# Performance work log

Measured on AMD Instinct MI355X. Metric: run time of the kernel, lower is better.

## Reference

```python
import jax, jax.numpy as jnp
import numpy as np

NEG_SLOPE = 0.2

def _leaky_relu(x):
    return jnp.where(x >= 0, x, NEG_SLOPE * x)

def setup_inputs() -> dict:
    key = jax.random.key(0)
    ks = jax.random.split(key, 12)
    B, N, M = 64, 4096, 128
    d_ope, d_ma, d_out = 6, 3, 8
    return {
        "ope_ma_adj": jax.random.randint(ks[0], (B, N, M), 0, 2, dtype=jnp.int32),
        "batch_idxes": jnp.arange(B, dtype=jnp.int32),
        "ope_feat": jax.random.normal(ks[1], (B, N, d_ope), dtype=jnp.float32),
        "ma_feat": jax.random.normal(ks[2], (B, M, d_ma), dtype=jnp.float32),
        "proc_time": jax.random.uniform(ks[3], (B, N, M), dtype=jnp.float32),
        "W_src": jax.random.normal(ks[4], (d_ope, d_out), dtype=jnp.float32),
        "W_dst": jax.random.normal(ks[5], (d_ma, d_out), dtype=jnp.float32),
        "w_edge": jax.random.normal(ks[6], (d_out,), dtype=jnp.float32),
        "attn_l": jax.random.normal(ks[7], (d_out,), dtype=jnp.float32),
        "attn_r": jax.random.normal(ks[8], (d_out,), dtype=jnp.float32),
        "attn_e": jax.random.normal(ks[9], (d_out,), dtype=jnp.float32),
    }

def reference(ope_ma_adj, batch_idxes, ope_feat, ma_feat, proc_time,
              W_src, W_dst, w_edge, attn_l, attn_r, attn_e):
    # GATedge.forward with num_head=1 (head dim folded away).
    adj_i = ope_ma_adj[batch_idxes]            # [B,N,M] int (0/1)
    adj = adj_i.astype(jnp.float32)
    feat_src = ope_feat @ W_src                # [B,N,d]
    feat_dst = ma_feat @ W_dst                 # [B,M,d]
    el = feat_src @ attn_l                     # [B,N]
    er = feat_dst @ attn_r                     # [B,M]
    # fc_edge is Linear(1,d): feat_edge = proc[...,None]*w_edge, so
    # ee = (feat_edge*attn_e).sum(-1) = proc * dot(w_edge, attn_e)
    ee = proc_time * jnp.dot(w_edge, attn_e)   # [B,N,M]
    a = adj * el[:, :, None] + ee + adj * er[:, None, :]
    eijk = _leaky_relu(a)                      # [B,N,M]
    ekk = _leaky_relu(2.0 * er)                # [B,M]
    neg_inf = jnp.asarray(-jnp.inf, dtype=eijk.dtype)
    eijk_m = jnp.where(adj_i == 1, eijk, neg_inf)
    e = jnp.concatenate([eijk_m, ekk[:, None, :]], axis=1)   # [B,N+1,M]
    alpha = jax.nn.softmax(e, axis=1)          # softmax over ops (+self)
    alpha_ijk = alpha[:, :-1, :]               # [B,N,M]
    alpha_kk = alpha[:, -1, :]                 # [B,M]
    # b = sum_j alpha_ijk * (feat_edge + feat_src), split to avoid [B,N,M,d]
    b_edge = jnp.einsum('bnm,bnm->bm', alpha_ijk, proc_time)[..., None] * w_edge  # [B,M,d]
    b_src = jnp.einsum('bnm,bnd->bmd', alpha_ijk, feat_src)                       # [B,M,d]
    c = feat_dst * alpha_kk[..., None]         # [B,M,d]
    return jax.nn.sigmoid(b_edge + b_src + c)  # nu_k_prime [B,M,d]
```

## Files before the change

### kernel.cpp

```cpp
#include <hip/hip_runtime.h>
#include <hip/hip_bf16.h>

constexpr int B  = 64;
constexpr int N  = 4096;
constexpr int M  = 128;
constexpr int DO = 8;
constexpr int NC = 32;
constexpr int CH = N / NC;
constexpr int RW = CH / 4;
constexpr int NS = RW / 2;
constexpr float CEXP = 20.0f;

constexpr int waitimm(int n) { return (n & 15) | ((n >> 4) << 14) | (7 << 4) | (15 << 8); }

typedef __attribute__((address_space(3))) void       lds_void;
typedef const __attribute__((address_space(1))) void gbl_void;

__global__ __launch_bounds__(256) void hgnn_k1(
    const int*   __restrict__ adj,
    const int*   __restrict__ bidx,
    const float* __restrict__ ope_feat,
    const float* __restrict__ ma_feat,
    const float* __restrict__ proc,
    const float* __restrict__ W_src,
    const float* __restrict__ W_dst,
    const float* __restrict__ w_edge,
    const float* __restrict__ attn_l,
    const float* __restrict__ attn_r,
    const float* __restrict__ attn_e,
    float*       __restrict__ acc)
{
    const int chunk = blockIdx.x;
    const int b     = blockIdx.y;
    const int t     = threadIdx.x;
    const int w     = t >> 6;
    const int lane  = t & 63;
    const int n0    = chunk * CH;

    __shared__ __align__(16) int   bufA[4][4][256];
    __shared__ __align__(16) float bufP[4][4][256];
    __shared__ __align__(16) float fs[CH][DO];
    __shared__ float el_s[CH];

    const int c0 = lane;
    const int c1 = lane + 64;

    float er0 = 0.f, er1 = 0.f, cee = 0.f;
    {
        const float* mf0 = ma_feat + ((size_t)b * M + c0) * 3;
        const float* mf1 = ma_feat + ((size_t)b * M + c1) * 3;
        const float a0 = mf0[0], a1 = mf0[1], a2 = mf0[2];
        const float b0 = mf1[0], b1 = mf1[1], b2 = mf1[2];
#pragma unroll
        for (int d = 0; d < DO; ++d) {
            er0 += (a0 * W_dst[d] + a1 * W_dst[DO + d] + a2 * W_dst[2 * DO + d]) * attn_r[d];
            er1 += (b0 * W_dst[d] + b1 * W_dst[DO + d] + b2 * W_dst[2 * DO + d]) * attn_r[d];
            cee += w_edge[d] * attn_e[d];
        }
    }

    if (t < CH) {
        const float* of = ope_feat + ((size_t)b * N + (n0 + t)) * 6;
        const float o0 = of[0], o1 = of[1], o2 = of[2], o3 = of[3], o4 = of[4], o5 = of[5];
        float el = 0.f;
#pragma unroll
        for (int d = 0; d < DO; ++d) {
            const float f = o0 * W_src[d] + o1 * W_src[DO + d] + o2 * W_src[2 * DO + d] +
                            o3 * W_src[3 * DO + d] + o4 * W_src[4 * DO + d] + o5 * W_src[5 * DO + d];
            fs[t][d] = f;
            el += f * attn_l[d];
        }
        el_s[t] = el;
    }
    __syncthreads();

    const int ab = bidx[b];
    const int*   adjw  = adj  + ((size_t)ab * N + n0 + w * RW) * M;
    const float* procw = proc + ((size_t)b  * N + n0 + w * RW) * M;
    const int l4 = lane * 4;

    auto issue = [&](int S) {
        __builtin_amdgcn_global_load_lds((gbl_void*)(adjw + (size_t)S * 256 + l4),
                                         (lds_void*)&bufA[w][S & 3][0], 16, 0, 0);
        __builtin_amdgcn_global_load_lds((gbl_void*)(procw + (size_t)S * 256 + l4),
                                         (lds_void*)&bufP[w][S & 3][0], 16, 0, 0);
    };

    float l0 = 0.f, sp0 = 0.f, l1 = 0.f, sp1 = 0.f;
    float sf0[DO], sf1[DO];
#pragma unroll
    for (int d = 0; d < DO; ++d) { sf0[d] = 0.f; sf1[d] = 0.f; }

    auto consume = [&](int S) {
        const int sb = (S & 3) * 256;
        const int* bA = &bufA[w][0][0];
        const float* bP = &bufP[w][0][0];
#pragma unroll
        for (int rr = 0; rr < 2; ++rr) {
            const int r = w * RW + S * 2 + rr;
            const float  el = el_s[r];
            const float4 f0 = *reinterpret_cast<const float4*>(&fs[r][0]);
            const float4 f1 = *reinterpret_cast<const float4*>(&fs[r][4]);
            const int   a0 = bA[sb + rr * 128 + c0];
            const int   a1 = bA[sb + rr * 128 + c1];
            const float p0 = bP[sb + rr * 128 + c0];
            const float p1 = bP[sb + rr * 128 + c1];
            {
                float v = el + er0 + cee * p0;
                v = (v >= 0.f) ? v : 0.2f * v;
                const float wt = __expf(((a0 != 0) ? v : -1e30f) - CEXP);
                l0 += wt; sp0 = fmaf(wt, p0, sp0);
                sf0[0] = fmaf(wt, f0.x, sf0[0]); sf0[1] = fmaf(wt, f0.y, sf0[1]);
                sf0[2] = fmaf(wt, f0.z, sf0[2]); sf0[3] = fmaf(wt, f0.w, sf0[3]);
                sf0[4] = fmaf(wt, f1.x, sf0[4]); sf0[5] = fmaf(wt, f1.y, sf0[5]);
                sf0[6] = fmaf(wt, f1.z, sf0[6]); sf0[7] = fmaf(wt, f1.w, sf0[7]);
            }
            {
                float v = el + er1 + cee * p1;
                v = (v >= 0.f) ? v : 0.2f * v;
                const float wt = __expf(((a1 != 0) ? v : -1e30f) - CEXP);
                l1 += wt; sp1 = fmaf(wt, p1, sp1);
                sf1[0] = fmaf(wt, f0.x, sf1[0]); sf1[1] = fmaf(wt, f0.y, sf1[1]);
                sf1[2] = fmaf(wt, f0.z, sf1[2]); sf1[3] = fmaf(wt, f0.w, sf1[3]);
                sf1[4] = fmaf(wt, f1.x, sf1[4]); sf1[5] = fmaf(wt, f1.y, sf1[5]);
                sf1[6] = fmaf(wt, f1.z, sf1[6]); sf1[7] = fmaf(wt, f1.w, sf1[7]);
            }
        }
    };

    issue(0); issue(1); issue(2); issue(3);

#define STEP_MI(S) { __builtin_amdgcn_s_waitcnt(waitimm(6)); consume(S); issue((S) + 4); }
#define STEP_NI(S, WN) { __builtin_amdgcn_s_waitcnt(waitimm(WN)); consume(S); }
    STEP_MI(0)  STEP_MI(1)  STEP_MI(2)  STEP_MI(3)
    STEP_MI(4)  STEP_MI(5)  STEP_MI(6)  STEP_MI(7)
    STEP_MI(8)  STEP_MI(9)  STEP_MI(10) STEP_MI(11)
    STEP_NI(12, 6) STEP_NI(13, 4) STEP_NI(14, 2) STEP_NI(15, 0)
#undef STEP_MI
#undef STEP_NI

    float* R = reinterpret_cast<float*>(&bufA[0][0][0]);
    const size_t colbase = (size_t)b * M;

    __syncthreads();
    {
        float v0[5] = {l0, sp0, sf0[0], sf0[1], sf0[2]};
        float v1[5] = {l1, sp1, sf1[0], sf1[1], sf1[2]};
#pragma unroll
        for (int k = 0; k < 5; ++k) {
            R[(w * 5 + k) * 128 + c0] = v0[k];
            R[(w * 5 + k) * 128 + c1] = v1[k];
        }
    }
    __syncthreads();
    if (t < M) {
#pragma unroll
        for (int k = 0; k < 5; ++k) {
            const float s = R[(0 * 5 + k) * 128 + t] + R[(1 * 5 + k) * 128 + t] +
                            R[(2 * 5 + k) * 128 + t] + R[(3 * 5 + k) * 128 + t];
            atomicAdd(&acc[(size_t)k * (B * M) + colbase + t], s);
        }
    }
    __syncthreads();
    {
        float v0[5] = {sf0[3], sf0[4], sf0[5], sf0[6], sf0[7]};
        float v1[5] = {sf1[3], sf1[4], sf1[5], sf1[6], sf1[7]};
#pragma unroll
        for (int k = 0; k < 5; ++k) {
            R[(w * 5 + k) * 128 + c0] = v0[k];
            R[(w * 5 + k) * 128 + c1] = v1[k];
        }
    }
    __syncthreads();
    if (t < M) {
#pragma unroll
        for (int k = 0; k < 5; ++k) {
            const float s = R[(0 * 5 + k) * 128 + t] + R[(1 * 5 + k) * 128 + t] +
                            R[(2 * 5 + k) * 128 + t] + R[(3 * 5 + k) * 128 + t];
            atomicAdd(&acc[(size_t)(5 + k) * (B * M) + colbase + t], s);
        }
    }
}

__global__ __launch_bounds__(256) void hgnn_k2(
    const float* __restrict__ ma_feat,
    const float* __restrict__ W_dst,
    const float* __restrict__ w_edge,
    const float* __restrict__ attn_r,
    const float* __restrict__ acc,
    float*       __restrict__ out)
{
    const int t = blockIdx.x * 256 + threadIdx.x;
    if (t >= B * M) return;
    const int m = t & (M - 1);
    const int b = t >> 7;

    float a[10];
#pragma unroll
    for (int f = 0; f < 10; ++f) a[f] = acc[(size_t)f * (B * M) + t];

    const float* mf = ma_feat + ((size_t)b * M + m) * 3;
    const float f0 = mf[0], f1 = mf[1], f2 = mf[2];
    float fd[DO];
    float er = 0.f;
#pragma unroll
    for (int d = 0; d < DO; ++d) {
        fd[d] = f0 * W_dst[d] + f1 * W_dst[DO + d] + f2 * W_dst[2 * DO + d];
        er += fd[d] * attn_r[d];
    }
    float ekk = 2.f * er;
    ekk = (ekk >= 0.f) ? ekk : 0.2f * ekk;
    const float wkk = __expf(ekk - CEXP);

    const float L    = a[0] + wkk;
    const float invL = 1.f / L;
    const float akk  = wkk * invL;
    const float spf  = a[1] * invL;

#pragma unroll
    for (int d = 0; d < DO; ++d) {
        const float x = spf * w_edge[d] + a[2 + d] * invL + fd[d] * akk;
        out[(size_t)t * DO + d] = 1.f / (1.f + __expf(-x));
    }
}

extern "C" void kernel_launch(void* const* d_in, const int* in_sizes, int n_in,
                              void* d_out, int out_size, void* d_ws, size_t ws_size,
                              hipStream_t stream) {
    const int*   adj      = (const int*)  d_in[0];
    const int*   bidx     = (const int*)  d_in[1];
    const float* ope_feat = (const float*)d_in[2];
    const float* ma_feat  = (const float*)d_in[3];
    const float* proc     = (const float*)d_in[4];
    const float* W_src    = (const float*)d_in[5];
    const float* W_dst    = (const float*)d_in[6];
    const float* w_edge   = (const float*)d_in[7];
    const float* attn_l   = (const float*)d_in[8];
    const float* attn_r   = (const float*)d_in[9];
    const float* attn_e   = (const float*)d_in[10];
    float* out = (float*)d_out;
    float* acc = (float*)d_ws;

    hipMemsetAsync(acc, 0, (size_t)10 * B * M * sizeof(float), stream);
    hgnn_k1<<<dim3(NC, B), 256, 0, stream>>>(adj, bidx, ope_feat, ma_feat, proc,
                                             W_src, W_dst, w_edge, attn_l, attn_r,
                                             attn_e, acc);
    hgnn_k2<<<dim3((B * M + 255) / 256), 256, 0, stream>>>(ma_feat, W_dst, w_edge,
                                                           attn_r, acc, out);
}
```

Before: 302.3 us.

## Replace LDS async staging with register-prefetched int2/float2 direct loads

Drops the global_load_lds ring buffer in LDS for adjacency and proc_time. Each lane now owns two adjacent columns and loads them as int2/float2 straight into registers, with a 4-deep software prefetch. This frees LDS and requests up to 8 blocks per CU via launch bounds, aiming for higher occupancy to hide memory latency. The masking is also simplified to select 0 after the exp, and leaky ReLU becomes fmaxf. The trade-off is narrower 8-byte loads per lane and more register pressure, where the old path used explicit 16-byte async copies.

```diff
diff --git a/kernel.cpp b/kernel.cpp
--- a/kernel.cpp
+++ b/kernel.cpp
@@ -1,5 +1,4 @@
 #include <hip/hip_runtime.h>
-#include <hip/hip_bf16.h>
 
 constexpr int B  = 64;
 constexpr int N  = 4096;
@@ -8,15 +7,10 @@
 constexpr int NC = 32;
 constexpr int CH = N / NC;
 constexpr int RW = CH / 4;
-constexpr int NS = RW / 2;
+constexpr int DP = 4;
 constexpr float CEXP = 20.0f;
 
-constexpr int waitimm(int n) { return (n & 15) | ((n >> 4) << 14) | (7 << 4) | (15 << 8); }
-
-typedef __attribute__((address_space(3))) void       lds_void;
-typedef const __attribute__((address_space(1))) void gbl_void;
-
-__global__ __launch_bounds__(256) void hgnn_k1(
+__global__ __launch_bounds__(256, 8) void hgnn_k1(
     const int*   __restrict__ adj,
     const int*   __restrict__ bidx,
     const float* __restrict__ ope_feat,
@@ -37,20 +31,17 @@
     const int lane  = t & 63;
     const int n0    = chunk * CH;
 
-    __shared__ __align__(16) int   bufA[4][4][256];
-    __shared__ __align__(16) float bufP[4][4][256];
     __shared__ __align__(16) float fs[CH][DO];
     __shared__ float el_s[CH];
-
-    const int c0 = lane;
-    const int c1 = lane + 64;
+    __shared__ float R[4][5][M];
+
+    const int c0 = lane * 2;
 
     float er0 = 0.f, er1 = 0.f, cee = 0.f;
     {
-        const float* mf0 = ma_feat + ((size_t)b * M + c0) * 3;
-        const float* mf1 = ma_feat + ((size_t)b * M + c1) * 3;
-        const float a0 = mf0[0], a1 = mf0[1], a2 = mf0[2];
-        const float b0 = mf1[0], b1 = mf1[1], b2 = mf1[2];
+        const float* mf = ma_feat + ((size_t)b * M + c0) * 3;
+        const float a0 = mf[0], a1 = mf[1], a2 = mf[2];
+        const float b0 = mf[3], b1 = mf[4], b2 = mf[5];
 #pragma unroll
         for (int d = 0; d < DO; ++d) {
             er0 += (a0 * W_dst[d] + a1 * W_dst[DO + d] + a2 * W_dst[2 * DO + d]) * attn_r[d];
@@ -75,71 +66,59 @@
     __syncthreads();
 
     const int ab = bidx[b];
-    const int*   adjw  = adj  + ((size_t)ab * N + n0 + w * RW) * M;
-    const float* procw = proc + ((size_t)b  * N + n0 + w * RW) * M;
-    const int l4 = lane * 4;
-
-    auto issue = [&](int S) {
-        __builtin_amdgcn_global_load_lds((gbl_void*)(adjw + (size_t)S * 256 + l4),
-                                         (lds_void*)&bufA[w][S & 3][0], 16, 0, 0);
-        __builtin_amdgcn_global_load_lds((gbl_void*)(procw + (size_t)S * 256 + l4),
-                                         (lds_void*)&bufP[w][S & 3][0], 16, 0, 0);
-    };
+    const int*   adjw  = adj  + ((size_t)ab * N + n0 + w * RW) * M + c0;
+    const float* procw = proc + ((size_t)b  * N + n0 + w * RW) * M + c0;
+
+    int2   Ab[DP];
+    float2 Pb[DP];
+#pragma unroll
+    for (int s = 0; s < DP; ++s) {
+        Ab[s] = *reinterpret_cast<const int2*>(adjw + (size_t)s * M);
+        Pb[s] = *reinterpret_cast<const float2*>(procw + (size_t)s * M);
+    }
 
     float l0 = 0.f, sp0 = 0.f, l1 = 0.f, sp1 = 0.f;
     float sf0[DO], sf1[DO];
 #pragma unroll
     for (int d = 0; d < DO; ++d) { sf0[d] = 0.f; sf1[d] = 0.f; }
 
-    auto consume = [&](int S) {
-        const int sb = (S & 3) * 256;
-        const int* bA = &bufA[w][0][0];
-        const float* bP = &bufP[w][0][0];
-#pragma unroll
-        for (int rr = 0; rr < 2; ++rr) {
-            const int r = w * RW + S * 2 + rr;
-            const float  el = el_s[r];
-            const float4 f0 = *reinterpret_cast<const float4*>(&fs[r][0]);
-            const float4 f1 = *reinterpret_cast<const float4*>(&fs[r][4]);
-            const int   a0 = bA[sb + rr * 128 + c0];
-            const int   a1 = bA[sb + rr * 128 + c1];
-            const float p0 = bP[sb + rr * 128 + c0];
-            const float p1 = bP[sb + rr * 128 + c1];
-            {
-                float v = el + er0 + cee * p0;
-                v = (v >= 0.f) ? v : 0.2f * v;
-                const float wt = __expf(((a0 != 0) ? v : -1e30f) - CEXP);
-                l0 += wt; sp0 = fmaf(wt, p0, sp0);
-                sf0[0] = fmaf(wt, f0.x, sf0[0]); sf0[1] = fmaf(wt, f0.y, sf0[1]);
-                sf0[2] = fmaf(wt, f0.z, sf0[2]); sf0[3] = fmaf(wt, f0.w, sf0[3]);
-                sf0[4] = fmaf(wt, f1.x, sf0[4]); sf0[5] = fmaf(wt, f1.y, sf0[5]);
-                sf0[6] = fmaf(wt, f1.z, sf0[6]); sf0[7] = fmaf(wt, f1.w, sf0[7]);
-            }
-            {
-                float v = el + er1 + cee * p1;
-                v = (v >= 0.f) ? v : 0.2f * v;
-                const float wt = __expf(((a1 != 0) ? v : -1e30f) - CEXP);
-                l1 += wt; sp1 = fmaf(wt, p1, sp1);
-                sf1[0] = fmaf(wt, f0.x, sf1[0]); sf1[1] = fmaf(wt, f0.y, sf1[1]);
-                sf1[2] = fmaf(wt, f0.z, sf1[2]); sf1[3] = fmaf(wt, f0.w, sf1[3]);
-                sf1[4] = fmaf(wt, f1.x, sf1[4]); sf1[5] = fmaf(wt, f1.y, sf1[5]);
-                sf1[6] = fmaf(wt, f1.z, sf1[6]); sf1[7] = fmaf(wt, f1.w, sf1[7]);
-            }
-        }
-    };
-
-    issue(0); issue(1); issue(2); issue(3);
-
-#define STEP_MI(S) { __builtin_amdgcn_s_waitcnt(waitimm(6)); consume(S); issue((S) + 4); }
-#define STEP_NI(S, WN) { __builtin_amdgcn_s_waitcnt(waitimm(WN)); consume(S); }
-    STEP_MI(0)  STEP_MI(1)  STEP_MI(2)  STEP_MI(3)
-    STEP_MI(4)  STEP_MI(5)  STEP_MI(6)  STEP_MI(7)
-    STEP_MI(8)  STEP_MI(9)  STEP_MI(10) STEP_MI(11)
-    STEP_NI(12, 6) STEP_NI(13, 4) STEP_NI(14, 2) STEP_NI(15, 0)
-#undef STEP_MI
-#undef STEP_NI
-
-    float* R = reinterpret_cast<float*>(&bufA[0][0][0]);
+#pragma unroll
+    for (int s = 0; s < RW; ++s) {
+        const int2   A = Ab[s & (DP - 1)];
+        const float2 P = Pb[s & (DP - 1)];
+        if (s + DP < RW) {
+            Ab[s & (DP - 1)] = *reinterpret_cast<const int2*>(adjw + (size_t)(s + DP) * M);
+            Pb[s & (DP - 1)] = *reinterpret_cast<const float2*>(procw + (size_t)(s + DP) * M);
+        }
+
+        const int r = w * RW + s;
+        const float  el = el_s[r];
+        const float4 f0 = *reinterpret_cast<const float4*>(&fs[r][0]);
+        const float4 f1 = *reinterpret_cast<const float4*>(&fs[r][4]);
+        {
+            float v = el + er0 + cee * P.x;
+            v = fmaxf(v, 0.2f * v);
+            const float e  = __expf(v - CEXP);
+            const float wt = (A.x != 0) ? e : 0.f;
+            l0 += wt; sp0 = fmaf(wt, P.x, sp0);
+            sf0[0] = fmaf(wt, f0.x, sf0[0]); sf0[1] = fmaf(wt, f0.y, sf0[1]);
+            sf0[2] = fmaf(wt, f0.z, sf0[2]); sf0[3] = fmaf(wt, f0.w, sf0[3]);
+            sf0[4] = fmaf(wt, f1.x, sf0[4]); sf0[5] = fmaf(wt, f1.y, sf0[5]);
+            sf0[6] = fmaf(wt, f1.z, sf0[6]); sf0[7] = fmaf(wt, f1.w, sf0[7]);
+        }
+        {
+            float v = el + er1 + cee * P.y;
+            v = fmaxf(v, 0.2f * v);
+            const float e  = __expf(v - CEXP);
+            const float wt = (A.y != 0) ? e : 0.f;
+            l1 += wt; sp1 = fmaf(wt, P.y, sp1);
+            sf1[0] = fmaf(wt, f0.x, sf1[0]); sf1[1] = fmaf(wt, f0.y, sf1[1]);
+            sf1[2] = fmaf(wt, f0.z, sf1[2]); sf1[3] = fmaf(wt, f0.w, sf1[3]);
+            sf1[4] = fmaf(wt, f1.x, sf1[4]); sf1[5] = fmaf(wt, f1.y, sf1[5]);
+            sf1[6] = fmaf(wt, f1.z, sf1[6]); sf1[7] = fmaf(wt, f1.w, sf1[7]);
+        }
+    }
+
     const size_t colbase = (size_t)b * M;
 
     __syncthreads();
@@ -148,16 +127,15 @@
         float v1[5] = {l1, sp1, sf1[0], sf1[1], sf1[2]};
 #pragma unroll
         for (int k = 0; k < 5; ++k) {
-            R[(w * 5 + k) * 128 + c0] = v0[k];
-            R[(w * 5 + k) * 128 + c1] = v1[k];
+            R[w][k][c0]     = v0[k];
+            R[w][k][c0 + 1] = v1[k];
         }
     }
     __syncthreads();
     if (t < M) {
 #pragma unroll
         for (int k = 0; k < 5; ++k) {
-            const float s = R[(0 * 5 + k) * 128 + t] + R[(1 * 5 + k) * 128 + t] +
-                            R[(2 * 5 + k) * 128 + t] + R[(3 * 5 + k) * 128 + t];
+            const float s = R[0][k][t] + R[1][k][t] + R[2][k][t] + R[3][k][t];
             atomicAdd(&acc[(size_t)k * (B * M) + colbase + t], s);
         }
     }
@@ -167,16 +145,15 @@
         float v1[5] = {sf1[3], sf1[4], sf1[5], sf1[6], sf1[7]};
 #pragma unroll
         for (int k = 0; k < 5; ++k) {
-            R[(w * 5 + k) * 128 + c0] = v0[k];
-            R[(w * 5 + k) * 128 + c1] = v1[k];
+            R[w][k][c0]     = v0[k];
+            R[w][k][c0 + 1] = v1[k];
         }
     }
     __syncthreads();
     if (t < M) {
 #pragma unroll
         for (int k = 0; k < 5; ++k) {
-            const float s = R[(0 * 5 + k) * 128 + t] + R[(1 * 5 + k) * 128 + t] +
-                            R[(2 * 5 + k) * 128 + t] + R[(3 * 5 + k) * 128 + t];
+            const float s = R[0][k][t] + R[1][k][t] + R[2][k][t] + R[3][k][t];
             atomicAdd(&acc[(size_t)(5 + k) * (B * M) + colbase + t], s);
         }
     }
```

Result: slower. 397.5 us (+31.5%).
